# Kernel optimization log

Measured on AMD Instinct MI355X. Metric: run time of the kernel, lower is better.

The kernel has to match this reference:

```python
import jax, jax.numpy as jnp
import numpy as np

EMB_DIM = 1024
N_EXPERTS = 8
TOP_K = 2
MOE_HIDDEN = 1024
NORM_TOPK = True


def setup_inputs() -> dict:
    key = jax.random.key(0)
    ks = jax.random.split(key, 7)
    s = 0.02
    return {
        "x": jax.random.normal(ks[0], (2, 2048, EMB_DIM), dtype=jnp.float32),
        "router_w": jax.random.normal(ks[1], (N_EXPERTS, EMB_DIM), dtype=jnp.float32) * s,
        "router_b": jnp.zeros((N_EXPERTS,), dtype=jnp.float32),
        "gate_up_w": jax.random.normal(ks[2], (N_EXPERTS, 2 * MOE_HIDDEN, EMB_DIM), dtype=jnp.float32) * s,
        "gate_up_b": jnp.zeros((N_EXPERTS, 2 * MOE_HIDDEN), dtype=jnp.float32),
        "down_w": jax.random.normal(ks[3], (N_EXPERTS, EMB_DIM, MOE_HIDDEN), dtype=jnp.float32) * s,
        "down_b": jnp.zeros((N_EXPERTS, EMB_DIM), dtype=jnp.float32),
    }


def _swiglu(h):
    # SwiGLUFFN: even columns gate, odd columns up
    gate = h[:, ::2]
    up = h[:, 1::2]
    return jnp.clip(gate, -7.0, 7.0) * jax.nn.sigmoid(1.702 * gate) * (jnp.clip(up, -7.0, 7.0) + 1.0)


def reference(x, router_w, router_b, gate_up_w, gate_up_b, down_w, down_b):
    B, S, D = x.shape
    h = x.reshape(B * S, D)  # [T, D]
    # Router: linear -> top-k -> (softmax over k)
    scores = h @ router_w.T + router_b  # [T, E]
    vals, idx = jax.lax.top_k(scores, TOP_K)  # [T, K]
    if NORM_TOPK:
        vals = jax.nn.softmax(vals, axis=-1)
    # Combine weights per (token, expert); zero for unselected experts, so
    # masked-dense compute below is mathematically identical to gather/scatter.
    cw = jnp.sum(jax.nn.one_hot(idx, N_EXPERTS, dtype=vals.dtype) * vals[..., None], axis=1)  # [T, E]
    out = jnp.zeros_like(h)
    for e in range(N_EXPERTS):  # fixed small expert count
        g = h @ gate_up_w[e].T + gate_up_b[e]  # [T, 2H]
        a = _swiglu(g)  # [T, H]
        oe = a @ down_w[e].T + down_b[e]  # [T, D]
        out = out + oe * cw[:, e:e + 1]
    return out.reshape(B, S, D)
```

## Files before the change

kernel.cpp:

```cpp
#include <hip/hip_runtime.h>
#include <hip/hip_bf16.h>

#define EMB 1024
#define NEXP 8
#define NH 1024
#define N_GU 2048
#define TOPK 2

#define BM 128
#define BN 128
#define BK 64
#define KTILES 16
#define MAXTILES 72

typedef __attribute__((ext_vector_type(4))) float f32x4;
typedef __attribute__((ext_vector_type(8))) short s16x8;
typedef __attribute__((ext_vector_type(4))) short s16x4;

typedef __attribute__((address_space(3))) unsigned int lds_u32;
typedef __attribute__((address_space(1))) const unsigned int glb_u32;

__device__ __forceinline__ void gl_lds16(const void* g, void* l) {
  __builtin_amdgcn_global_load_lds((glb_u32*)g, (lds_u32*)l, 16, 0, 0);
}

__device__ __forceinline__ unsigned short f2bf(float f) {
  union { float f; unsigned int u; } a; a.f = f;
  unsigned int u = a.u;
  unsigned int r = (u + 0x7FFFu + ((u >> 16) & 1u)) >> 16;
  return (unsigned short)r;
}

__device__ __forceinline__ float b2f(unsigned short h) {
  union { unsigned int u; float f; } a;
  a.u = ((unsigned int)h) << 16;
  return a.f;
}

__device__ __forceinline__ int xcd_swz(int bid, int nwg) {
  int q = nwg >> 3, r = nwg & 7;
  int xcd = bid & 7, pos = bid >> 3;
  int base = (xcd < r) ? xcd * (q + 1) : r * (q + 1) + (xcd - r) * q;
  return base + pos;
}

__global__ void convert_router(const float* __restrict__ x, unsigned short* __restrict__ xb, int n4x,
                               const float* __restrict__ guw, unsigned short* __restrict__ guwb, int n4g,
                               const float* __restrict__ dw, unsigned short* __restrict__ dwb, int n4d,
                               const float* __restrict__ rw, const float* __restrict__ rb, int T,
                               int* __restrict__ tokE, float* __restrict__ tokW) {
  int nr = T / 4;
  if ((int)blockIdx.x < nr) {
    int gwid = blockIdx.x * 4 + (threadIdx.x >> 6);
    int lane = threadIdx.x & 63;
    if (gwid >= T) return;
    const float* h = x + (size_t)gwid * EMB;
    float hreg[16];
    #pragma unroll
    for (int i = 0; i < 16; ++i) hreg[i] = h[lane + 64 * i];
    float sc[NEXP];
    #pragma unroll
    for (int e = 0; e < NEXP; ++e) {
      const float* w = rw + e * EMB;
      float s = 0.f;
      #pragma unroll
      for (int i = 0; i < 16; ++i) s += hreg[i] * w[lane + 64 * i];
      #pragma unroll
      for (int off = 32; off > 0; off >>= 1) s += __shfl_xor(s, off);
      sc[e] = s + rb[e];
    }
    if (lane == 0) {
      int e0 = 0; float v0 = sc[0];
      #pragma unroll
      for (int e = 1; e < NEXP; ++e) if (sc[e] > v0) { v0 = sc[e]; e0 = e; }
      int e1 = -1; float v1 = -3.0e38f;
      #pragma unroll
      for (int e = 0; e < NEXP; ++e) { if (e == e0) continue; if (sc[e] > v1) { v1 = sc[e]; e1 = e; } }
      float ex = __expf(v1 - v0);
      float w0 = 1.f / (1.f + ex);
      float w1 = ex / (1.f + ex);
      tokE[gwid * 2] = e0; tokE[gwid * 2 + 1] = e1;
      tokW[gwid * 2] = w0; tokW[gwid * 2 + 1] = w1;
    }
  } else {
    int tot = n4x + n4g + n4d;
    int base = (blockIdx.x - nr) * blockDim.x + threadIdx.x;
    int stride = (gridDim.x - nr) * blockDim.x;
    for (int i = base; i < tot; i += stride) {
      const float* src; unsigned short* dst; int k;
      if (i < n4x) { src = x; dst = xb; k = i; }
      else if (i < n4x + n4g) { src = guw; dst = guwb; k = i - n4x; }
      else { src = dw; dst = dwb; k = i - n4x - n4g; }
      float4 v = ((const float4*)src)[k];
      s16x4 o;
      o[0] = (short)f2bf(v.x);
      o[1] = (short)f2bf(v.y);
      o[2] = (short)f2bf(v.z);
      o[3] = (short)f2bf(v.w);
      ((s16x4*)dst)[k] = o;
    }
  }
}

__global__ void count_meta(const int* __restrict__ tokE, int A,
                           int* __restrict__ offsets, int* __restrict__ tilemeta) {
  __shared__ int hist[NEXP];
  int t = threadIdx.x;
  if (t < NEXP) hist[t] = 0;
  __syncthreads();
  for (int i = t; i < A; i += blockDim.x) atomicAdd(&hist[tokE[i]], 1);
  __syncthreads();
  if (t == 0) {
    int off = 0, nt = 0;
    for (int e = 0; e < NEXP; ++e) {
      offsets[e] = off;
      int c = hist[e];
      int ntile = (c + BM - 1) / BM;
      for (int k = 0; k < ntile; ++k) {
        tilemeta[1 + nt * 3 + 0] = e;
        tilemeta[1 + nt * 3 + 1] = off + k * BM;
        tilemeta[1 + nt * 3 + 2] = off + c;
        nt++;
      }
      off += c;
    }
    offsets[NEXP] = off;
    tilemeta[0] = nt;
  }
}

__global__ void scatter_tokens(const int* __restrict__ tokE, const int* __restrict__ offsets,
                               int* __restrict__ fill, int* __restrict__ rows,
                               int* __restrict__ apos, int A) {
  int i = blockIdx.x * blockDim.x + threadIdx.x;
  int lane = threadIdx.x & 63;
  int e = tokE[i];
  int p = -1;
  #pragma unroll
  for (int ex = 0; ex < NEXP; ++ex) {
    unsigned long long mask = __ballot(e == ex);
    if (mask) {
      int leader = __ffsll(mask) - 1;
      int cnt = __popcll(mask);
      int base = 0;
      if (lane == leader) base = atomicAdd(&fill[ex], cnt);
      base = __shfl(base, leader);
      if (e == ex) {
        int rank = __popcll(mask & ((1ull << lane) - 1ull));
        p = offsets[ex] + base + rank;
      }
    }
  }
  rows[p] = i >> 1;
  apos[i] = p;
}

__global__ __launch_bounds__(256, 4) void gemm_gate_up(
    const unsigned short* __restrict__ xb,
    const unsigned short* __restrict__ gub,
    const float* __restrict__ gu_bias,
    const int* __restrict__ rows,
    const int* __restrict__ tilemeta,
    unsigned short* __restrict__ hact) {
  __shared__ __align__(16) short As[BM * BK];
  __shared__ __align__(16) short Bs[BN * BK];
  int wg = xcd_swz(blockIdx.x, gridDim.x);
  int tileid = wg >> 4;
  int n0 = (wg & 15) * BN;
  int nt = tilemeta[0];
  if (tileid >= nt) return;
  int e    = tilemeta[1 + tileid * 3 + 0];
  int m0   = tilemeta[1 + tileid * 3 + 1];
  int mEnd = tilemeta[1 + tileid * 3 + 2];

  int t = threadIdx.x;
  int lane = t & 63;
  int wid = t >> 6;
  int wr = wid >> 1, wc = wid & 1;

  int srow = lane >> 3;
  int scol = (((lane & 7) ^ (srow & 7)) * 8);
  const unsigned short* ga[4];
  const unsigned short* gb[4];
  int dstoff[4];
  #pragma unroll
  for (int q = 0; q < 4; ++q) {
    int rt = wid * 32 + q * 8 + srow;
    int ai = m0 + rt; if (ai >= mEnd) ai = mEnd - 1;
    ga[q] = xb + (size_t)rows[ai] * EMB + scol;
    gb[q] = gub + ((size_t)e * N_GU + n0 + rt) * EMB + scol;
    dstoff[q] = (wid * 32 + q * 8) * BK;
  }

  int fr = lane & 15;
  int q8 = (lane >> 4) * 8;
  int rsw = (fr & 7) << 3;

  f32x4 acc[4][4];
  #pragma unroll
  for (int i = 0; i < 4; ++i)
    #pragma unroll
    for (int j = 0; j < 4; ++j) acc[i][j] = (f32x4){0.f, 0.f, 0.f, 0.f};

  for (int tk = 0; tk < KTILES; ++tk) {
    int k0 = tk * BK;
    __syncthreads();
    #pragma unroll
    for (int q = 0; q < 4; ++q) {
      gl_lds16(ga[q] + k0, &As[dstoff[q]]);
      gl_lds16(gb[q] + k0, &Bs[dstoff[q]]);
    }
    __syncthreads();
    #pragma unroll
    for (int kk = 0; kk < BK; kk += 32) {
      s16x8 a[4], b[4];
      #pragma unroll
      for (int i = 0; i < 4; ++i)
        a[i] = *(const s16x8*)(&As[(wr * 64 + i * 16 + fr) * BK + ((kk + q8) ^ rsw)]);
      #pragma unroll
      for (int j = 0; j < 4; ++j)
        b[j] = *(const s16x8*)(&Bs[(wc * 64 + j * 16 + fr) * BK + ((kk + q8) ^ rsw)]);
      #pragma unroll
      for (int i = 0; i < 4; ++i)
        #pragma unroll
        for (int j = 0; j < 4; ++j)
          acc[i][j] = __builtin_amdgcn_mfma_f32_16x16x32_bf16(a[i], b[j], acc[i][j], 0, 0, 0);
    }
  }

  const float* bias_e = gu_bias + (size_t)e * N_GU;
  int rbase = m0 + wr * 64 + ((lane >> 4) * 4);
  #pragma unroll
  for (int i = 0; i < 4; ++i) {
    #pragma unroll
    for (int j = 0; j < 4; ++j) {
      int n = n0 + wc * 64 + j * 16 + fr;
      float v[4], o[4];
      #pragma unroll
      for (int r = 0; r < 4; ++r) v[r] = acc[i][j][r] + bias_e[n];
      #pragma unroll
      for (int r = 0; r < 4; ++r) o[r] = __shfl_xor(v[r], 1);
      if ((lane & 1) == 0) {
        int outc = n >> 1;
        #pragma unroll
        for (int r = 0; r < 4; ++r) {
          int pos = rbase + i * 16 + r;
          if (pos < mEnd) {
            float g = v[r], u = o[r];
            float gc = fminf(fmaxf(g, -7.f), 7.f);
            float uc = fminf(fmaxf(u, -7.f), 7.f);
            float sig = 1.f / (1.f + __expf(-1.702f * g));
            float act = gc * sig * (uc + 1.f);
            hact[(size_t)pos * NH + outc] = f2bf(act);
          }
        }
      }
    }
  }
}

__global__ __launch_bounds__(256, 4) void gemm_down(
    const unsigned short* __restrict__ hact,
    const unsigned short* __restrict__ dwb,
    const int* __restrict__ tilemeta,
    unsigned short* __restrict__ y) {
  __shared__ __align__(16) short As[BM * BK];
  __shared__ __align__(16) short Bs[BN * BK];
  int wg = xcd_swz(blockIdx.x, gridDim.x);
  int tileid = wg >> 3;
  int n0 = (wg & 7) * BN;
  int nt = tilemeta[0];
  if (tileid >= nt) return;
  int e    = tilemeta[1 + tileid * 3 + 0];
  int m0   = tilemeta[1 + tileid * 3 + 1];
  int mEnd = tilemeta[1 + tileid * 3 + 2];

  int t = threadIdx.x;
  int lane = t & 63;
  int wid = t >> 6;
  int wr = wid >> 1, wc = wid & 1;

  int srow = lane >> 3;
  int scol = (((lane & 7) ^ (srow & 7)) * 8);
  const unsigned short* ga[4];
  const unsigned short* gb[4];
  int dstoff[4];
  #pragma unroll
  for (int q = 0; q < 4; ++q) {
    int rt = wid * 32 + q * 8 + srow;
    int ai = m0 + rt; if (ai >= mEnd) ai = mEnd - 1;
    ga[q] = hact + (size_t)ai * NH + scol;
    gb[q] = dwb + ((size_t)e * EMB + n0 + rt) * NH + scol;
    dstoff[q] = (wid * 32 + q * 8) * BK;
  }

  int fr = lane & 15;
  int q8 = (lane >> 4) * 8;
  int rsw = (fr & 7) << 3;

  f32x4 acc[4][4];
  #pragma unroll
  for (int i = 0; i < 4; ++i)
    #pragma unroll
    for (int j = 0; j < 4; ++j) acc[i][j] = (f32x4){0.f, 0.f, 0.f, 0.f};

  for (int tk = 0; tk < KTILES; ++tk) {
    int k0 = tk * BK;
    __syncthreads();
    #pragma unroll
    for (int q = 0; q < 4; ++q) {
      gl_lds16(ga[q] + k0, &As[dstoff[q]]);
      gl_lds16(gb[q] + k0, &Bs[dstoff[q]]);
    }
    __syncthreads();
    #pragma unroll
    for (int kk = 0; kk < BK; kk += 32) {
      s16x8 a[4], b[4];
      #pragma unroll
      for (int i = 0; i < 4; ++i)
        a[i] = *(const s16x8*)(&As[(wr * 64 + i * 16 + fr) * BK + ((kk + q8) ^ rsw)]);
      #pragma unroll
      for (int j = 0; j < 4; ++j)
        b[j] = *(const s16x8*)(&Bs[(wc * 64 + j * 16 + fr) * BK + ((kk + q8) ^ rsw)]);
      #pragma unroll
      for (int i = 0; i < 4; ++i)
        #pragma unroll
        for (int j = 0; j < 4; ++j)
          acc[i][j] = __builtin_amdgcn_mfma_f32_16x16x32_bf16(a[i], b[j], acc[i][j], 0, 0, 0);
    }
  }

  int rbase = m0 + wr * 64 + ((lane >> 4) * 4);
  #pragma unroll
  for (int i = 0; i < 4; ++i) {
    #pragma unroll
    for (int j = 0; j < 4; ++j) {
      int n = n0 + wc * 64 + j * 16 + fr;
      #pragma unroll
      for (int r = 0; r < 4; ++r) {
        int pos = rbase + i * 16 + r;
        if (pos < mEnd) y[(size_t)pos * EMB + n] = f2bf(acc[i][j][r]);
      }
    }
  }
}

__global__ void combine_out(const unsigned short* __restrict__ y, const float* __restrict__ down_b,
                            const int* __restrict__ tokE, const float* __restrict__ tokW,
                            const int* __restrict__ apos, float* __restrict__ out, int T) {
  int i = blockIdx.x * blockDim.x + threadIdx.x;
  int tot = T * (EMB / 4);
  if (i >= tot) return;
  int tok = i >> 8;
  int c = i & 255;
  int e0 = tokE[tok * 2], e1 = tokE[tok * 2 + 1];
  float w0 = tokW[tok * 2], w1 = tokW[tok * 2 + 1];
  int p0 = apos[tok * 2], p1 = apos[tok * 2 + 1];
  s16x4 v0 = ((const s16x4*)(y + (size_t)p0 * EMB))[c];
  s16x4 v1 = ((const s16x4*)(y + (size_t)p1 * EMB))[c];
  float4 b0 = ((const float4*)(down_b + (size_t)e0 * EMB))[c];
  float4 b1 = ((const float4*)(down_b + (size_t)e1 * EMB))[c];
  float4 o;
  o.x = w0 * (b2f((unsigned short)v0[0]) + b0.x) + w1 * (b2f((unsigned short)v1[0]) + b1.x);
  o.y = w0 * (b2f((unsigned short)v0[1]) + b0.y) + w1 * (b2f((unsigned short)v1[1]) + b1.y);
  o.z = w0 * (b2f((unsigned short)v0[2]) + b0.z) + w1 * (b2f((unsigned short)v1[2]) + b1.z);
  o.w = w0 * (b2f((unsigned short)v0[3]) + b0.w) + w1 * (b2f((unsigned short)v1[3]) + b1.w);
  ((float4*)out)[i] = o;
}

extern "C" void kernel_launch(void* const* d_in, const int* in_sizes, int n_in,
                              void* d_out, int out_size, void* d_ws, size_t ws_size,
                              hipStream_t stream) {
  const float* x   = (const float*)d_in[0];
  const float* rw  = (const float*)d_in[1];
  const float* rb  = (const float*)d_in[2];
  const float* guw = (const float*)d_in[3];
  const float* gub = (const float*)d_in[4];
  const float* dw  = (const float*)d_in[5];
  const float* db  = (const float*)d_in[6];
  float* out = (float*)d_out;

  int T = in_sizes[0] / EMB;
  int A = T * TOPK;

  char* ws = (char*)d_ws;
  size_t off = 0;
  auto alloc = [&](size_t bytes) -> void* {
    void* p = ws + off;
    off = (off + bytes + 255) & ~((size_t)255);
    return p;
  };
  unsigned short* xb   = (unsigned short*)alloc((size_t)T * EMB * 2);
  unsigned short* guwb = (unsigned short*)alloc((size_t)NEXP * N_GU * EMB * 2);
  unsigned short* dwb  = (unsigned short*)alloc((size_t)NEXP * EMB * NH * 2);
  unsigned short* hact = (unsigned short*)alloc((size_t)A * NH * 2);
  unsigned short* y    = (unsigned short*)alloc((size_t)A * EMB * 2);
  int*   tokE    = (int*)alloc((size_t)A * 4);
  float* tokW    = (float*)alloc((size_t)A * 4);
  int*   apos    = (int*)alloc((size_t)A * 4);
  int*   rowsArr = (int*)alloc((size_t)A * 4);
  int*   fill    = (int*)alloc(NEXP * 4);
  int*   offsets = (int*)alloc((NEXP + 1) * 4);
  int*   tilemeta= (int*)alloc((1 + MAXTILES * 3) * 4);

  hipMemsetAsync(fill, 0, NEXP * 4, stream);

  int n4x = T * EMB / 4;
  int n4g = NEXP * N_GU * EMB / 4;
  int n4d = NEXP * EMB * NH / 4;
  convert_router<<<T / 4 + 2048, 256, 0, stream>>>(x, xb, n4x, guw, guwb, n4g, dw, dwb, n4d,
                                                   rw, rb, T, tokE, tokW);

  count_meta<<<1, 1024, 0, stream>>>(tokE, A, offsets, tilemeta);
  scatter_tokens<<<A / 256, 256, 0, stream>>>(tokE, offsets, fill, rowsArr, apos, A);

  gemm_gate_up<<<MAXTILES * (N_GU / BN), 256, 0, stream>>>(xb, guwb, gub, rowsArr, tilemeta, hact);
  gemm_down<<<MAXTILES * (EMB / BN), 256, 0, stream>>>(hact, dwb, tilemeta, y);

  combine_out<<<(T * EMB / 4 + 255) / 256, 256, 0, stream>>>(y, db, tokE, tokW, apos, out, T);
}
```

Measured before the change: 154.0 us.

## Double-buffer LDS in expert GEMMs and overlap down-weight conversion with gate-up GEMM

Both expert GEMMs now use a double-buffered LDS pipeline with BK=32. The next K-slice is fetched via global_load_lds while MFMAs run on the current one, and there is one barrier per step instead of two. The fp32-to-bf16 conversion of the down-projection weights moves out of the first conversion kernel into extra workgroups appended to the gate-up GEMM launch, so it overlaps with GEMM work. The costs are twice as many pipeline iterations, a modified LDS swizzle, and conversion blocks competing with the GEMM for bandwidth.

```diff
diff --git a/kernel.cpp b/kernel.cpp
--- a/kernel.cpp
+++ b/kernel.cpp
@@ -9,9 +9,11 @@
 
 #define BM 128
 #define BN 128
-#define BK 64
-#define KTILES 16
+#define BK 32
+#define NSUB 32
 #define MAXTILES 72
+#define GRID_GU (MAXTILES * 16)
+#define CONV_BLKS 256
 
 typedef __attribute__((ext_vector_type(4))) float f32x4;
 typedef __attribute__((ext_vector_type(8))) short s16x8;
@@ -22,6 +24,12 @@
 
 __device__ __forceinline__ void gl_lds16(const void* g, void* l) {
   __builtin_amdgcn_global_load_lds((glb_u32*)g, (lds_u32*)l, 16, 0, 0);
+}
+
+__device__ __forceinline__ void barrier_fence() {
+  asm volatile("" ::: "memory");
+  __builtin_amdgcn_s_barrier();
+  asm volatile("" ::: "memory");
 }
 
 __device__ __forceinline__ unsigned short f2bf(float f) {
@@ -46,7 +54,6 @@
 
 __global__ void convert_router(const float* __restrict__ x, unsigned short* __restrict__ xb, int n4x,
                                const float* __restrict__ guw, unsigned short* __restrict__ guwb, int n4g,
-                               const float* __restrict__ dw, unsigned short* __restrict__ dwb, int n4d,
                                const float* __restrict__ rw, const float* __restrict__ rb, int T,
                                int* __restrict__ tokE, float* __restrict__ tokW) {
   int nr = T / 4;
@@ -83,14 +90,13 @@
       tokW[gwid * 2] = w0; tokW[gwid * 2 + 1] = w1;
     }
   } else {
-    int tot = n4x + n4g + n4d;
+    int tot = n4x + n4g;
     int base = (blockIdx.x - nr) * blockDim.x + threadIdx.x;
     int stride = (gridDim.x - nr) * blockDim.x;
     for (int i = base; i < tot; i += stride) {
       const float* src; unsigned short* dst; int k;
       if (i < n4x) { src = x; dst = xb; k = i; }
-      else if (i < n4x + n4g) { src = guw; dst = guwb; k = i - n4x; }
-      else { src = dw; dst = dwb; k = i - n4x - n4g; }
+      else { src = guw; dst = guwb; k = i - n4x; }
       float4 v = ((const float4*)src)[k];
       s16x4 o;
       o[0] = (short)f2bf(v.x);
@@ -161,10 +167,25 @@
     const float* __restrict__ gu_bias,
     const int* __restrict__ rows,
     const int* __restrict__ tilemeta,
-    unsigned short* __restrict__ hact) {
-  __shared__ __align__(16) short As[BM * BK];
-  __shared__ __align__(16) short Bs[BN * BK];
-  int wg = xcd_swz(blockIdx.x, gridDim.x);
+    unsigned short* __restrict__ hact,
+    const float* __restrict__ dw, unsigned short* __restrict__ dwb, int n4d) {
+  __shared__ __align__(16) short As[2][BM * BK];
+  __shared__ __align__(16) short Bs[2][BN * BK];
+  if ((int)blockIdx.x >= GRID_GU) {
+    int base = ((int)blockIdx.x - GRID_GU) * blockDim.x + threadIdx.x;
+    int stride = CONV_BLKS * blockDim.x;
+    for (int i = base; i < n4d; i += stride) {
+      float4 v = ((const float4*)dw)[i];
+      s16x4 o;
+      o[0] = (short)f2bf(v.x);
+      o[1] = (short)f2bf(v.y);
+      o[2] = (short)f2bf(v.z);
+      o[3] = (short)f2bf(v.w);
+      ((s16x4*)dwb)[i] = o;
+    }
+    return;
+  }
+  int wg = xcd_swz(blockIdx.x, GRID_GU);
   int tileid = wg >> 4;
   int n0 = (wg & 15) * BN;
   int nt = tilemeta[0];
@@ -178,23 +199,23 @@
   int wid = t >> 6;
   int wr = wid >> 1, wc = wid & 1;
 
-  int srow = lane >> 3;
-  int scol = (((lane & 7) ^ (srow & 7)) * 8);
-  const unsigned short* ga[4];
-  const unsigned short* gb[4];
-  int dstoff[4];
-  #pragma unroll
-  for (int q = 0; q < 4; ++q) {
-    int rt = wid * 32 + q * 8 + srow;
+  int srow = lane >> 2;
+  int scol = (((lane & 3) ^ ((lane >> 3) & 3)) * 8);
+  const unsigned short* ga[2];
+  const unsigned short* gb[2];
+  int dstoff[2];
+  #pragma unroll
+  for (int q = 0; q < 2; ++q) {
+    int rt = q * 64 + wid * 16 + srow;
     int ai = m0 + rt; if (ai >= mEnd) ai = mEnd - 1;
     ga[q] = xb + (size_t)rows[ai] * EMB + scol;
     gb[q] = gub + ((size_t)e * N_GU + n0 + rt) * EMB + scol;
-    dstoff[q] = (wid * 32 + q * 8) * BK;
+    dstoff[q] = (q * 64 + wid * 16) * BK;
   }
 
   int fr = lane & 15;
-  int q8 = (lane >> 4) * 8;
-  int rsw = (fr & 7) << 3;
+  int kq = (lane >> 4) * 8;
+  int rsw = ((fr & 7) >> 1) << 3;
 
   f32x4 acc[4][4];
   #pragma unroll
@@ -202,29 +223,39 @@
     #pragma unroll
     for (int j = 0; j < 4; ++j) acc[i][j] = (f32x4){0.f, 0.f, 0.f, 0.f};
 
-  for (int tk = 0; tk < KTILES; ++tk) {
-    int k0 = tk * BK;
-    __syncthreads();
-    #pragma unroll
-    for (int q = 0; q < 4; ++q) {
-      gl_lds16(ga[q] + k0, &As[dstoff[q]]);
-      gl_lds16(gb[q] + k0, &Bs[dstoff[q]]);
-    }
-    __syncthreads();
-    #pragma unroll
-    for (int kk = 0; kk < BK; kk += 32) {
-      s16x8 a[4], b[4];
-      #pragma unroll
-      for (int i = 0; i < 4; ++i)
-        a[i] = *(const s16x8*)(&As[(wr * 64 + i * 16 + fr) * BK + ((kk + q8) ^ rsw)]);
+  #pragma unroll
+  for (int q = 0; q < 2; ++q) {
+    gl_lds16(ga[q], &As[0][dstoff[q]]);
+    gl_lds16(gb[q], &Bs[0][dstoff[q]]);
+  }
+  asm volatile("s_waitcnt vmcnt(0)" ::: "memory");
+  barrier_fence();
+
+  for (int tk = 0; tk < NSUB; ++tk) {
+    int cur = tk & 1;
+    if (tk + 1 < NSUB) {
+      int k0 = (tk + 1) * BK;
+      #pragma unroll
+      for (int q = 0; q < 2; ++q) {
+        gl_lds16(ga[q] + k0, &As[cur ^ 1][dstoff[q]]);
+        gl_lds16(gb[q] + k0, &Bs[cur ^ 1][dstoff[q]]);
+      }
+    }
+    s16x8 a[4], b[4];
+    #pragma unroll
+    for (int i = 0; i < 4; ++i)
+      a[i] = *(const s16x8*)(&As[cur][(wr * 64 + i * 16 + fr) * BK + (kq ^ rsw)]);
+    #pragma unroll
+    for (int j = 0; j < 4; ++j)
+      b[j] = *(const s16x8*)(&Bs[cur][(wc * 64 + j * 16 + fr) * BK + (kq ^ rsw)]);
+    #pragma unroll
+    for (int i = 0; i < 4; ++i)
       #pragma unroll
       for (int j = 0; j < 4; ++j)
-        b[j] = *(const s16x8*)(&Bs[(wc * 64 + j * 16 + fr) * BK + ((kk + q8) ^ rsw)]);
-      #pragma unroll
-      for (int i = 0; i < 4; ++i)
-        #pragma unroll
-        for (int j = 0; j < 4; ++j)
-          acc[i][j] = __builtin_amdgcn_mfma_f32_16x16x32_bf16(a[i], b[j], acc[i][j], 0, 0, 0);
+        acc[i][j] = __builtin_amdgcn_mfma_f32_16x16x32_bf16(a[i], b[j], acc[i][j], 0, 0, 0);
+    if (tk + 1 < NSUB) {
+      asm volatile("s_waitcnt vmcnt(0)" ::: "memory");
+      barrier_fence();
     }
   }
 
@@ -264,8 +295,8 @@
     const unsigned short* __restrict__ dwb,
     const int* __restrict__ tilemeta,
     unsigned short* __restrict__ y) {
-  __shared__ __align__(16) short As[BM * BK];
-  __shared__ __align__(16) short Bs[BN * BK];
+  __shared__ __align__(16) short As[2][BM * BK];
+  __shared__ __align__(16) short Bs[2][BN * BK];
   int wg = xcd_swz(blockIdx.x, gridDim.x);
   int tileid = wg >> 3;
   int n0 = (wg & 7) * BN;
@@ -280,23 +311,23 @@
   int wid = t >> 6;
   int wr = wid >> 1, wc = wid & 1;
 
-  int srow = lane >> 3;
-  int scol = (((lane & 7) ^ (srow & 7)) * 8);
-  const unsigned short* ga[4];
-  const unsigned short* gb[4];
-  int dstoff[4];
-  #pragma unroll
-  for (int q = 0; q < 4; ++q) {
-    int rt = wid * 32 + q * 8 + srow;
+  int srow = lane >> 2;
+  int scol = (((lane & 3) ^ ((lane >> 3) & 3)) * 8);
+  const unsigned short* ga[2];
+  const unsigned short* gb[2];
+  int dstoff[2];
+  #pragma unroll
+  for (int q = 0; q < 2; ++q) {
+    int rt = q * 64 + wid * 16 + srow;
     int ai = m0 + rt; if (ai >= mEnd) ai = mEnd - 1;
     ga[q] = hact + (size_t)ai * NH + scol;
     gb[q] = dwb + ((size_t)e * EMB + n0 + rt) * NH + scol;
-    dstoff[q] = (wid * 32 + q * 8) * BK;
+    dstoff[q] = (q * 64 + wid * 16) * BK;
   }
 
   int fr = lane & 15;
-  int q8 = (lane >> 4) * 8;
-  int rsw = (fr & 7) << 3;
+  int kq = (lane >> 4) * 8;
+  int rsw = ((fr & 7) >> 1) << 3;
 
   f32x4 acc[4][4];
   #pragma unroll
@@ -304,29 +335,39 @@
     #pragma unroll
     for (int j = 0; j < 4; ++j) acc[i][j] = (f32x4){0.f, 0.f, 0.f, 0.f};
 
-  for (int tk = 0; tk < KTILES; ++tk) {
-    int k0 = tk * BK;
-    __syncthreads();
-    #pragma unroll
-    for (int q = 0; q < 4; ++q) {
-      gl_lds16(ga[q] + k0, &As[dstoff[q]]);
-      gl_lds16(gb[q] + k0, &Bs[dstoff[q]]);
-    }
-    __syncthreads();
-    #pragma unroll
-    for (int kk = 0; kk < BK; kk += 32) {
-      s16x8 a[4], b[4];
-      #pragma unroll
-      for (int i = 0; i < 4; ++i)
-        a[i] = *(const s16x8*)(&As[(wr * 64 + i * 16 + fr) * BK + ((kk + q8) ^ rsw)]);
+  #pragma unroll
+  for (int q = 0; q < 2; ++q) {
+    gl_lds16(ga[q], &As[0][dstoff[q]]);
+    gl_lds16(gb[q], &Bs[0][dstoff[q]]);
+  }
+  asm volatile("s_waitcnt vmcnt(0)" ::: "memory");
+  barrier_fence();
+
+  for (int tk = 0; tk < NSUB; ++tk) {
+    int cur = tk & 1;
+    if (tk + 1 < NSUB) {
+      int k0 = (tk + 1) * BK;
+      #pragma unroll
+      for (int q = 0; q < 2; ++q) {
+        gl_lds16(ga[q] + k0, &As[cur ^ 1][dstoff[q]]);
+        gl_lds16(gb[q] + k0, &Bs[cur ^ 1][dstoff[q]]);
+      }
+    }
+    s16x8 a[4], b[4];
+    #pragma unroll
+    for (int i = 0; i < 4; ++i)
+      a[i] = *(const s16x8*)(&As[cur][(wr * 64 + i * 16 + fr) * BK + (kq ^ rsw)]);
+    #pragma unroll
+    for (int j = 0; j < 4; ++j)
+      b[j] = *(const s16x8*)(&Bs[cur][(wc * 64 + j * 16 + fr) * BK + (kq ^ rsw)]);
+    #pragma unroll
+    for (int i = 0; i < 4; ++i)
       #pragma unroll
       for (int j = 0; j < 4; ++j)
-        b[j] = *(const s16x8*)(&Bs[(wc * 64 + j * 16 + fr) * BK + ((kk + q8) ^ rsw)]);
-      #pragma unroll
-      for (int i = 0; i < 4; ++i)
-        #pragma unroll
-        for (int j = 0; j < 4; ++j)
-          acc[i][j] = __builtin_amdgcn_mfma_f32_16x16x32_bf16(a[i], b[j], acc[i][j], 0, 0, 0);
+        acc[i][j] = __builtin_amdgcn_mfma_f32_16x16x32_bf16(a[i], b[j], acc[i][j], 0, 0, 0);
+    if (tk + 1 < NSUB) {
+      asm volatile("s_waitcnt vmcnt(0)" ::: "memory");
+      barrier_fence();
     }
   }
 
@@ -408,13 +449,14 @@
   int n4x = T * EMB / 4;
   int n4g = NEXP * N_GU * EMB / 4;
   int n4d = NEXP * EMB * NH / 4;
-  convert_router<<<T / 4 + 2048, 256, 0, stream>>>(x, xb, n4x, guw, guwb, n4g, dw, dwb, n4d,
+  convert_router<<<T / 4 + 2048, 256, 0, stream>>>(x, xb, n4x, guw, guwb, n4g,
                                                    rw, rb, T, tokE, tokW);
 
   count_meta<<<1, 1024, 0, stream>>>(tokE, A, offsets, tilemeta);
   scatter_tokens<<<A / 256, 256, 0, stream>>>(tokE, offsets, fill, rowsArr, apos, A);
 
-  gemm_gate_up<<<MAXTILES * (N_GU / BN), 256, 0, stream>>>(xb, guwb, gub, rowsArr, tilemeta, hact);
+  gemm_gate_up<<<GRID_GU + CONV_BLKS, 256, 0, stream>>>(xb, guwb, gub, rowsArr, tilemeta, hact,
+                                                        dw, dwb, n4d);
   gemm_down<<<MAXTILES * (EMB / BN), 256, 0, stream>>>(hact, dwb, tilemeta, y);
 
   combine_out<<<(T * EMB / 4 + 255) / 256, 256, 0, stream>>>(y, db, tokE, tokW, apos, out, T);
```

After: 163.4 us. +6.1%, slower.
